# Optimization experiments

Hardware: AMD Instinct MI355X
Metric: run time of the kernel (lower is better)

## Reference

```python
import jax, jax.numpy as jnp
import numpy as np
from jax import lax

EPS = 1e-5
KS = 3
PAD = 1
C = 256
G = 8          # ska_groups
VG = 8         # verifier groups
B, H, W = 8, 128, 128


def _bn(y, gamma, beta, mean, var):
    # inference-mode BatchNorm2d
    inv = gamma / jnp.sqrt(var + EPS)
    return y * inv[None, :, None, None] + (beta - mean * inv)[None, :, None, None]


def setup_inputs() -> dict:
    key = jax.random.key(0)
    ks = jax.random.split(key, 12)
    x = jax.random.normal(ks[0], (B, C, H, W), jnp.float32)
    dynamic_weight = jax.random.normal(ks[1], (B, G, KS * KS, H, W), jnp.float32)
    roi_mask = jax.random.uniform(ks[2], (B, 1, H, W), jnp.float32)
    # local_verifier params: Conv2d_BN(C,C,ks=3,pad=1,groups=8) -> ReLU -> Conv2d_BN(C,C,ks=1)
    w1 = jax.random.normal(ks[3], (C, C // VG, 3, 3), jnp.float32) * 0.05
    g1 = jnp.ones((C,), jnp.float32)
    b1 = jnp.zeros((C,), jnp.float32)
    m1 = jax.random.normal(ks[4], (C,), jnp.float32) * 0.1
    v1 = jax.random.uniform(ks[5], (C,), jnp.float32) + 0.5
    w2 = jax.random.normal(ks[6], (C, C, 1, 1), jnp.float32) * 0.05
    g2 = jnp.ones((C,), jnp.float32)
    b2 = jnp.zeros((C,), jnp.float32)
    m2 = jax.random.normal(ks[7], (C,), jnp.float32) * 0.1
    v2 = jax.random.uniform(ks[8], (C,), jnp.float32) + 0.5
    return dict(x=x, dynamic_weight=dynamic_weight, roi_mask=roi_mask,
                w1=w1, g1=g1, b1=b1, m1=m1, v1=v1,
                w2=w2, g2=g2, b2=b2, m2=m2, v2=v2)


def reference(x, dynamic_weight, roi_mask, w1, g1, b1, m1, v1, w2, g2, b2, m2, v2):
    Bx, Cx, Hx, Wx = x.shape
    gc = Cx // G  # group_channels
    # SKA: spatially-varying 3x3 aggregation. Boundary-dependent slicing in the
    # original is equivalent to zero-padding x by PAD.
    x_pad = jnp.pad(x, ((0, 0), (0, 0), (PAD, PAD), (PAD, PAD)))
    xg = x_pad.reshape(Bx, G, gc, Hx + 2 * PAD, Wx + 2 * PAD)
    ska = jnp.zeros((Bx, G, gc, Hx, Wx), x.dtype)
    for kh in range(KS):
        for kw in range(KS):
            ska = ska + xg[:, :, :, kh:kh + Hx, kw:kw + Wx] * \
                  dynamic_weight[:, :, None, kh * KS + kw]
    ska = ska.reshape(Bx, Cx, Hx, Wx)
    # local verifier: grouped 3x3 conv + BN + ReLU + 1x1 conv + BN
    y = ska * roi_mask
    y = lax.conv_general_dilated(y, w1, (1, 1), 'SAME',
                                 feature_group_count=VG,
                                 dimension_numbers=('NCHW', 'OIHW', 'NCHW'))
    y = jax.nn.relu(_bn(y, g1, b1, m1, v1))
    y = lax.conv_general_dilated(y, w2, (1, 1), 'VALID',
                                 dimension_numbers=('NCHW', 'OIHW', 'NCHW'))
    y = _bn(y, g2, b2, m2, v2)
    return ska + y
```

## Files before the change

kernel.cpp:

```cpp
#include <hip/hip_runtime.h>
#include <hip/hip_bf16.h>


#define HW 16384
#define EPS 1e-5f

typedef __bf16 bf16x8 __attribute__((ext_vector_type(8)));
typedef short short8 __attribute__((ext_vector_type(8)));
typedef short short4v __attribute__((ext_vector_type(4)));
typedef float floatx4 __attribute__((ext_vector_type(4)));

__device__ __forceinline__ unsigned short f2bf(float f) {
  unsigned u = __builtin_bit_cast(unsigned, f);
  unsigned r = u + 0x7FFFu + ((u >> 16) & 1u);
  return (unsigned short)(r >> 16);
}

__device__ __forceinline__ floatx4 mfma16(short8 a, short8 b, floatx4 c) {
  return __builtin_amdgcn_mfma_f32_16x16x32_bf16(
      __builtin_bit_cast(bf16x8, a), __builtin_bit_cast(bf16x8, b), c, 0, 0, 0);
}

__global__ __launch_bounds__(256) void prepack(const float* __restrict__ w1,
                                               const float* __restrict__ w2,
                                               unsigned short* __restrict__ w1b,
                                               unsigned short* __restrict__ w2b) {
  int o = blockIdx.x * 256 + threadIdx.x;
  if (o < 73728) {
    int ci  = o & 31;
    int co  = (o >> 5) & 31;
    int khw = (o >> 10) % 9;
    int g   = (o >> 10) / 9;
    w1b[o] = f2bf(w1[((g * 32 + co) * 32 + ci) * 9 + khw]);
  } else {
    int p = o - 73728;
    w2b[p] = f2bf(w2[p]);
  }
}

__global__ __launch_bounds__(256) void ska_kernel(const float* __restrict__ x,
                                                  const float* __restrict__ dw,
                                                  const float* __restrict__ roi,
                                                  float* __restrict__ out,
                                                  unsigned short* __restrict__ y0b) {
  __shared__ unsigned short tile[32 * 36];

  int phys = blockIdx.x;
  int blk  = (phys & 7) * 4096 + (phys >> 3);
  int wt = blk & 3;
  int h  = (blk >> 2) & 127;
  int g  = (blk >> 9) & 7;
  int b  = blk >> 12;
  int tid = threadIdx.x;
  int ci = tid >> 3;
  int wq = tid & 7;
  int w0 = wt * 32 + wq * 4;
  int c  = g * 32 + ci;

  size_t base = ((size_t)(b * 256 + c)) * HW + h * 128 + w0;
  const float* dwb = dw + ((size_t)(b * 8 + g) * 9) * HW + h * 128 + w0;

  floatx4 wv[9];
#pragma unroll
  for (int k = 0; k < 9; ++k) wv[k] = *(const floatx4*)&dwb[k * HW];

  float xr[3][6];
#pragma unroll
  for (int kh = 0; kh < 3; ++kh) {
    int hh = h + kh - 1;
    if ((unsigned)hh < 128u) {
      const float* xp = x + base + (kh - 1) * 128;
      floatx4 m = *(const floatx4*)xp;
      xr[kh][0] = (w0 > 0) ? xp[-1] : 0.f;
      xr[kh][1] = m[0];
      xr[kh][2] = m[1];
      xr[kh][3] = m[2];
      xr[kh][4] = m[3];
      xr[kh][5] = (w0 < 124) ? xp[4] : 0.f;
    } else {
#pragma unroll
      for (int i = 0; i < 6; ++i) xr[kh][i] = 0.f;
    }
  }

  floatx4 rv = *(const floatx4*)&roi[(size_t)b * HW + h * 128 + w0];

  float s[4] = {0.f, 0.f, 0.f, 0.f};
#pragma unroll
  for (int kh = 0; kh < 3; ++kh) {
#pragma unroll
    for (int kw = 0; kw < 3; ++kw) {
      floatx4 wk = wv[kh * 3 + kw];
#pragma unroll
      for (int j = 0; j < 4; ++j) s[j] += xr[kh][kw + j] * wk[j];
    }
  }

  *(floatx4*)&out[base] = (floatx4){s[0], s[1], s[2], s[3]};

  int wl = wq * 4;
#pragma unroll
  for (int j = 0; j < 4; ++j)
    tile[(wl + j) * 36 + ci] = f2bf(s[j] * rv[j]);

  __syncthreads();

  unsigned short* dst =
      y0b + ((size_t)(b * 8 + g) * HW + h * 128 + wt * 32) * 32;
  int w = tid >> 3, k = tid & 7;
  *(short4v*)&dst[tid * 4] = *(const short4v*)&tile[w * 36 + k * 4];
}

__global__ __launch_bounds__(256) void conv1_mfma(
    const unsigned short* __restrict__ y0, const unsigned short* __restrict__ w1b,
    const float* __restrict__ g1, const float* __restrict__ b1,
    const float* __restrict__ m1, const float* __restrict__ v1,
    unsigned short* __restrict__ h1t) {
  __shared__ unsigned short xt[324 * 40];

  int blk  = blockIdx.x;
  int tile = blk & 63;
  int g    = (blk >> 6) & 7;
  int b    = blk >> 9;
  int h0   = (tile >> 3) * 16;
  int w0   = (tile & 7) * 16;
  int tid  = threadIdx.x;

  const unsigned short* xsrc = y0 + (size_t)(b * 8 + g) * HW * 32;
  for (int j = tid; j < 1296; j += 256) {
    int r = j >> 2, part = j & 3;
    int yy = r / 18, xx = r - yy * 18;
    int gh = h0 - 1 + yy, gw = w0 - 1 + xx;
    short8 v = (short8){0, 0, 0, 0, 0, 0, 0, 0};
    if ((unsigned)gh < 128u && (unsigned)gw < 128u)
      v = *(const short8*)&xsrc[(size_t)(gh * 128 + gw) * 32 + part * 8];
    *(short8*)&xt[r * 40 + part * 8] = v;
  }

  int wv = tid >> 6, lane = tid & 63, q = lane >> 4, n = lane & 15;

  short8 bf[9][2];
  const unsigned short* wgb = w1b + (size_t)g * 9 * 32 * 32;
#pragma unroll
  for (int khw = 0; khw < 9; ++khw) {
#pragma unroll
    for (int half = 0; half < 2; ++half)
      bf[khw][half] =
          *(const short8*)&wgb[(khw * 32 + half * 16 + n) * 32 + q * 8];
  }

  __syncthreads();

  floatx4 acc[4][2];
#pragma unroll
  for (int r = 0; r < 4; ++r)
#pragma unroll
    for (int half = 0; half < 2; ++half) acc[r][half] = (floatx4){0.f, 0.f, 0.f, 0.f};

#pragma unroll
  for (int r = 0; r < 4; ++r) {
    int row = wv * 4 + r;
#pragma unroll
    for (int khw = 0; khw < 9; ++khw) {
      int kh = khw / 3, kw = khw % 3;
      short8 a = *(const short8*)&xt[((row + kh) * 18 + kw + n) * 40 + q * 8];
      acc[r][0] = mfma16(a, bf[khw][0], acc[r][0]);
      acc[r][1] = mfma16(a, bf[khw][1], acc[r][1]);
    }
  }

  float inv[2], bias[2];
#pragma unroll
  for (int half = 0; half < 2; ++half) {
    int c = g * 32 + half * 16 + n;
    inv[half]  = g1[c] * rsqrtf(v1[c] + EPS);
    bias[half] = b1[c] - m1[c] * inv[half];
  }

  __syncthreads();

#pragma unroll
  for (int r = 0; r < 4; ++r) {
    int pr = (wv * 4 + r) * 16;
#pragma unroll
    for (int half = 0; half < 2; ++half) {
      int co = half * 16 + n;
#pragma unroll
      for (int reg = 0; reg < 4; ++reg) {
        int px = pr + q * 4 + reg;
        float v = fmaxf(acc[r][half][reg] * inv[half] + bias[half], 0.f);
        xt[px * 40 + co] = f2bf(v);
      }
    }
  }

  __syncthreads();

  unsigned short* hb = h1t + (size_t)(b * 8 + g) * HW * 32;
  int ph = tid >> 4, pw = tid & 15;
  size_t gp = (size_t)((h0 + ph) * 128 + (w0 + pw)) * 32;
#pragma unroll
  for (int k = 0; k < 4; ++k)
    *(short8*)&hb[gp + k * 8] = *(const short8*)&xt[tid * 40 + k * 8];
}

__global__ __launch_bounds__(256) void conv2_mfma(
    const unsigned short* __restrict__ h1t, const unsigned short* __restrict__ w2b,
    const float* __restrict__ g2, const float* __restrict__ b2,
    const float* __restrict__ m2, const float* __restrict__ v2,
    float* __restrict__ out) {
  int blk = blockIdx.x;
  int b   = blk >> 8;
  int px0 = (blk & 255) * 64;
  int tid = threadIdx.x;
  int wv = tid >> 6, lane = tid & 63, q = lane >> 4, n = lane & 15;

  floatx4 acc[4][4];
#pragma unroll
  for (int mt = 0; mt < 4; ++mt)
#pragma unroll
    for (int nt = 0; nt < 4; ++nt) acc[mt][nt] = (floatx4){0.f, 0.f, 0.f, 0.f};

  for (int s = 0; s < 8; ++s) {
    short8 a[4];
#pragma unroll
    for (int mt = 0; mt < 4; ++mt)
      a[mt] = *(const short8*)&h1t[((size_t)(b * 8 + s) * HW + px0 + mt * 16 + n) * 32 +
                                   q * 8];
#pragma unroll
    for (int nt = 0; nt < 4; ++nt) {
      int co = wv * 64 + nt * 16 + n;
      short8 bb = *(const short8*)&w2b[co * 256 + s * 32 + q * 8];
#pragma unroll
      for (int mt = 0; mt < 4; ++mt) acc[mt][nt] = mfma16(a[mt], bb, acc[mt][nt]);
    }
  }

#pragma unroll
  for (int nt = 0; nt < 4; ++nt) {
    int co = wv * 64 + nt * 16 + n;
    float inv  = g2[co] * rsqrtf(v2[co] + EPS);
    float bias = b2[co] - m2[co] * inv;
    float* ob = out + (size_t)(b * 256 + co) * HW;
#pragma unroll
    for (int mt = 0; mt < 4; ++mt) {
      int px = px0 + mt * 16 + q * 4;
      float4 sv = *(float4*)&ob[px];
      sv.x += acc[mt][nt][0] * inv + bias;
      sv.y += acc[mt][nt][1] * inv + bias;
      sv.z += acc[mt][nt][2] * inv + bias;
      sv.w += acc[mt][nt][3] * inv + bias;
      *(float4*)&ob[px] = sv;
    }
  }
}

extern "C" void kernel_launch(void* const* d_in, const int* in_sizes, int n_in,
                              void* d_out, int out_size, void* d_ws,
                              size_t ws_size, hipStream_t stream) {
  const float* x   = (const float*)d_in[0];
  const float* dw  = (const float*)d_in[1];
  const float* roi = (const float*)d_in[2];
  const float* w1  = (const float*)d_in[3];
  const float* g1  = (const float*)d_in[4];
  const float* b1  = (const float*)d_in[5];
  const float* m1  = (const float*)d_in[6];
  const float* v1  = (const float*)d_in[7];
  const float* w2  = (const float*)d_in[8];
  const float* g2  = (const float*)d_in[9];
  const float* b2  = (const float*)d_in[10];
  const float* m2  = (const float*)d_in[11];
  const float* v2  = (const float*)d_in[12];
  float* out = (float*)d_out;

  char* ws = (char*)d_ws;
  unsigned short* y0b = (unsigned short*)ws;
  unsigned short* h1t = (unsigned short*)(ws + 67108864);
  unsigned short* w1b = (unsigned short*)(ws + 134217728);
  unsigned short* w2b = (unsigned short*)(ws + 134365184);

  prepack<<<544, 256, 0, stream>>>(w1, w2, w1b, w2b);
  ska_kernel<<<32768, 256, 0, stream>>>(x, dw, roi, out, y0b);
  conv1_mfma<<<4096, 256, 0, stream>>>(y0b, w1b, g1, b1, m1, v1, h1t);
  conv2_mfma<<<2048, 256, 0, stream>>>(h1t, w2b, g2, b2, m2, v2, out);
}
```

Before: 534.0 us.

## Process two rows per SKA block, batch conv1 loads, pipeline conv2 via LDS

The SKA kernel now handles two output rows per block. It stages the dynamic weights and ROI mask in shared memory and reuses the four loaded input rows across both outputs, which cuts redundant x reads. conv1 issues all its tile loads before any LDS stores so more memory requests are in flight at once. conv2 streams activation slices into a triple-buffered LDS ring with asynchronous global-to-LDS loads, overlapping the fetches with MFMA work at the cost of extra barriers and shared memory.

Measured after the change: 459.8 us. 13.9% less time.

```diff
diff --git a/kernel.cpp b/kernel.cpp
--- a/kernel.cpp
+++ b/kernel.cpp
@@ -38,77 +38,87 @@
   }
 }
 
-__global__ __launch_bounds__(256) void ska_kernel(const float* __restrict__ x,
-                                                  const float* __restrict__ dw,
-                                                  const float* __restrict__ roi,
-                                                  float* __restrict__ out,
-                                                  unsigned short* __restrict__ y0b) {
-  __shared__ unsigned short tile[32 * 36];
+__global__ __launch_bounds__(256, 4) void ska_kernel(
+    const float* __restrict__ x, const float* __restrict__ dw,
+    const float* __restrict__ roi, float* __restrict__ out,
+    unsigned short* __restrict__ y0b) {
+  __shared__ float dwf[9][2][32];
+  __shared__ float roib[2][32];
+  __shared__ unsigned short tile[2 * 32 * 36];
 
   int phys = blockIdx.x;
-  int blk  = (phys & 7) * 4096 + (phys >> 3);
+  int blk  = (phys & 7) * 2048 + (phys >> 3);
   int wt = blk & 3;
-  int h  = (blk >> 2) & 127;
-  int g  = (blk >> 9) & 7;
-  int b  = blk >> 12;
+  int hp = (blk >> 2) & 63;
+  int g  = (blk >> 8) & 7;
+  int b  = blk >> 11;
+  int h0 = hp * 2;
   int tid = threadIdx.x;
   int ci = tid >> 3;
   int wq = tid & 7;
   int w0 = wt * 32 + wq * 4;
   int c  = g * 32 + ci;
 
-  size_t base = ((size_t)(b * 256 + c)) * HW + h * 128 + w0;
-  const float* dwb = dw + ((size_t)(b * 8 + g) * 9) * HW + h * 128 + w0;
-
-  floatx4 wv[9];
-#pragma unroll
-  for (int k = 0; k < 9; ++k) wv[k] = *(const floatx4*)&dwb[k * HW];
-
-  float xr[3][6];
-#pragma unroll
-  for (int kh = 0; kh < 3; ++kh) {
-    int hh = h + kh - 1;
+  if (tid < 160) {
+    if (tid < 144) {
+      int k = tid >> 4, r = (tid >> 3) & 1, w4 = (tid & 7) * 4;
+      *(floatx4*)&dwf[k][r][w4] = *(const floatx4*)
+          &dw[((size_t)(b * 8 + g) * 9 + k) * HW + (h0 + r) * 128 + wt * 32 + w4];
+    } else {
+      int i = tid - 144, r = i >> 3, w4 = (i & 7) * 4;
+      *(floatx4*)&roib[r][w4] = *(const floatx4*)
+          &roi[(size_t)b * HW + (h0 + r) * 128 + wt * 32 + w4];
+    }
+  }
+
+  float xr[4][6];
+#pragma unroll
+  for (int rr = 0; rr < 4; ++rr) {
+    int hh = h0 - 1 + rr;
     if ((unsigned)hh < 128u) {
-      const float* xp = x + base + (kh - 1) * 128;
+      const float* xp = &x[((size_t)(b * 256 + c)) * HW + hh * 128 + w0];
       floatx4 m = *(const floatx4*)xp;
-      xr[kh][0] = (w0 > 0) ? xp[-1] : 0.f;
-      xr[kh][1] = m[0];
-      xr[kh][2] = m[1];
-      xr[kh][3] = m[2];
-      xr[kh][4] = m[3];
-      xr[kh][5] = (w0 < 124) ? xp[4] : 0.f;
+      xr[rr][0] = (w0 > 0) ? xp[-1] : 0.f;
+      xr[rr][1] = m[0];
+      xr[rr][2] = m[1];
+      xr[rr][3] = m[2];
+      xr[rr][4] = m[3];
+      xr[rr][5] = (w0 < 124) ? xp[4] : 0.f;
     } else {
 #pragma unroll
-      for (int i = 0; i < 6; ++i) xr[kh][i] = 0.f;
-    }
-  }
-
-  floatx4 rv = *(const floatx4*)&roi[(size_t)b * HW + h * 128 + w0];
-
-  float s[4] = {0.f, 0.f, 0.f, 0.f};
-#pragma unroll
-  for (int kh = 0; kh < 3; ++kh) {
-#pragma unroll
-    for (int kw = 0; kw < 3; ++kw) {
-      floatx4 wk = wv[kh * 3 + kw];
-#pragma unroll
-      for (int j = 0; j < 4; ++j) s[j] += xr[kh][kw + j] * wk[j];
-    }
-  }
-
-  *(floatx4*)&out[base] = (floatx4){s[0], s[1], s[2], s[3]};
-
-  int wl = wq * 4;
-#pragma unroll
-  for (int j = 0; j < 4; ++j)
-    tile[(wl + j) * 36 + ci] = f2bf(s[j] * rv[j]);
+      for (int i = 0; i < 6; ++i) xr[rr][i] = 0.f;
+    }
+  }
+
+  __syncthreads();
+
+  size_t base = ((size_t)(b * 256 + c)) * HW + h0 * 128 + w0;
+#pragma unroll
+  for (int r = 0; r < 2; ++r) {
+    float s[4] = {0.f, 0.f, 0.f, 0.f};
+#pragma unroll
+    for (int kh = 0; kh < 3; ++kh)
+#pragma unroll
+      for (int kw = 0; kw < 3; ++kw) {
+        floatx4 wk = *(const floatx4*)&dwf[kh * 3 + kw][r][wq * 4];
+#pragma unroll
+        for (int j = 0; j < 4; ++j) s[j] += xr[r + kh][kw + j] * wk[j];
+      }
+    *(floatx4*)&out[base + r * 128] = (floatx4){s[0], s[1], s[2], s[3]};
+    floatx4 rv = *(const floatx4*)&roib[r][wq * 4];
+#pragma unroll
+    for (int j = 0; j < 4; ++j)
+      tile[(r * 32 + wq * 4 + j) * 36 + ci] = f2bf(s[j] * rv[j]);
+  }
 
   __syncthreads();
 
   unsigned short* dst =
-      y0b + ((size_t)(b * 8 + g) * HW + h * 128 + wt * 32) * 32;
-  int w = tid >> 3, k = tid & 7;
-  *(short4v*)&dst[tid * 4] = *(const short4v*)&tile[w * 36 + k * 4];
+      y0b + ((size_t)(b * 8 + g) * HW + h0 * 128 + wt * 32) * 32;
+  int row = tid >> 7, rest = tid & 127;
+  int w = rest >> 2, kk = rest & 3;
+  *(short8*)&dst[(size_t)row * 128 * 32 + w * 32 + kk * 8] =
+      *(const short8*)&tile[(row * 32 + w) * 36 + kk * 8];
 }
 
 __global__ __launch_bounds__(256) void conv1_mfma(
@@ -127,14 +137,27 @@
   int tid  = threadIdx.x;
 
   const unsigned short* xsrc = y0 + (size_t)(b * 8 + g) * HW * 32;
-  for (int j = tid; j < 1296; j += 256) {
-    int r = j >> 2, part = j & 3;
-    int yy = r / 18, xx = r - yy * 18;
-    int gh = h0 - 1 + yy, gw = w0 - 1 + xx;
+  short8 sv[6];
+#pragma unroll
+  for (int t = 0; t < 6; ++t) {
+    int j = tid + t * 256;
     short8 v = (short8){0, 0, 0, 0, 0, 0, 0, 0};
-    if ((unsigned)gh < 128u && (unsigned)gw < 128u)
-      v = *(const short8*)&xsrc[(size_t)(gh * 128 + gw) * 32 + part * 8];
-    *(short8*)&xt[r * 40 + part * 8] = v;
+    if (j < 1296) {
+      int r = j >> 2, part = j & 3;
+      int yy = r / 18, xx = r - yy * 18;
+      int gh = h0 - 1 + yy, gw = w0 - 1 + xx;
+      if ((unsigned)gh < 128u && (unsigned)gw < 128u)
+        v = *(const short8*)&xsrc[(size_t)(gh * 128 + gw) * 32 + part * 8];
+    }
+    sv[t] = v;
+  }
+#pragma unroll
+  for (int t = 0; t < 6; ++t) {
+    int j = tid + t * 256;
+    if (j < 1296) {
+      int r = j >> 2, part = j & 3;
+      *(short8*)&xt[r * 40 + part * 8] = sv[t];
+    }
   }
 
   int wv = tid >> 6, lane = tid & 63, q = lane >> 4, n = lane & 15;
@@ -172,9 +195,9 @@
   float inv[2], bias[2];
 #pragma unroll
   for (int half = 0; half < 2; ++half) {
-    int c = g * 32 + half * 16 + n;
-    inv[half]  = g1[c] * rsqrtf(v1[c] + EPS);
-    bias[half] = b1[c] - m1[c] * inv[half];
+    int cc = g * 32 + half * 16 + n;
+    inv[half]  = g1[cc] * rsqrtf(v1[cc] + EPS);
+    bias[half] = b1[cc] - m1[cc] * inv[half];
   }
 
   __syncthreads();
@@ -209,32 +232,54 @@
     const float* __restrict__ g2, const float* __restrict__ b2,
     const float* __restrict__ m2, const float* __restrict__ v2,
     float* __restrict__ out) {
+  __shared__ unsigned short As[3][2048];
+
   int blk = blockIdx.x;
   int b   = blk >> 8;
   int px0 = (blk & 255) * 64;
   int tid = threadIdx.x;
   int wv = tid >> 6, lane = tid & 63, q = lane >> 4, n = lane & 15;
 
+  const unsigned short* sb = h1t + ((size_t)b * 8 * HW + px0) * 32;
+
+#define STAGE(S, BUF)                                                         \
+  __builtin_amdgcn_global_load_lds(                                           \
+      (const __attribute__((address_space(1))) unsigned int*)(sb +            \
+          (size_t)(S) * HW * 32 + wv * 512 + lane * 8),                       \
+      (__attribute__((address_space(3))) unsigned int*)&As[BUF][wv * 512],    \
+      16, 0, 0)
+
   floatx4 acc[4][4];
 #pragma unroll
   for (int mt = 0; mt < 4; ++mt)
 #pragma unroll
     for (int nt = 0; nt < 4; ++nt) acc[mt][nt] = (floatx4){0.f, 0.f, 0.f, 0.f};
 
+  STAGE(0, 0);
+  STAGE(1, 1);
+  asm volatile("s_waitcnt vmcnt(1)");
+  __syncthreads();
+
+#pragma unroll
   for (int s = 0; s < 8; ++s) {
-    short8 a[4];
-#pragma unroll
-    for (int mt = 0; mt < 4; ++mt)
-      a[mt] = *(const short8*)&h1t[((size_t)(b * 8 + s) * HW + px0 + mt * 16 + n) * 32 +
-                                   q * 8];
-#pragma unroll
-    for (int nt = 0; nt < 4; ++nt) {
-      int co = wv * 64 + nt * 16 + n;
-      short8 bb = *(const short8*)&w2b[co * 256 + s * 32 + q * 8];
-#pragma unroll
-      for (int mt = 0; mt < 4; ++mt) acc[mt][nt] = mfma16(a[mt], bb, acc[mt][nt]);
-    }
-  }
+    if (s < 6) STAGE(s + 2, (s + 2) % 3);
+    short8 bb[4];
+#pragma unroll
+    for (int nt = 0; nt < 4; ++nt)
+      bb[nt] =
+          *(const short8*)&w2b[(wv * 64 + nt * 16 + n) * 256 + s * 32 + q * 8];
+    const unsigned short* Ab = &As[s % 3][0];
+#pragma unroll
+    for (int mt = 0; mt < 4; ++mt) {
+      short8 a = *(const short8*)&Ab[(mt * 16 + n) * 32 + q * 8];
+#pragma unroll
+      for (int nt = 0; nt < 4; ++nt) acc[mt][nt] = mfma16(a, bb[nt], acc[mt][nt]);
+    }
+    if (s < 6) asm volatile("s_waitcnt vmcnt(1)");
+    else if (s == 6) asm volatile("s_waitcnt vmcnt(0)");
+    if (s < 7) __syncthreads();
+  }
+#undef STAGE
 
 #pragma unroll
   for (int nt = 0; nt < 4; ++nt) {
@@ -280,7 +325,7 @@
   unsigned short* w2b = (unsigned short*)(ws + 134365184);
 
   prepack<<<544, 256, 0, stream>>>(w1, w2, w1b, w2b);
-  ska_kernel<<<32768, 256, 0, stream>>>(x, dw, roi, out, y0b);
+  ska_kernel<<<16384, 256, 0, stream>>>(x, dw, roi, out, y0b);
   conv1_mfma<<<4096, 256, 0, stream>>>(y0b, w1b, g1, b1, m1, v1, h1t);
   conv2_mfma<<<2048, 256, 0, stream>>>(h1t, w2b, g2, b2, m2, v2, out);
 }
```
